# Optimization experiments

Measured on AMD Instinct MI355X. Metric: run time of the kernel, lower is better.

## Reference

```python
import jax, jax.numpy as jnp
import numpy as np
from jax import lax

ALPHA, BETA, THR = 0.9, 0.85, 1.0
NUM_STEPS = 100

@jax.custom_vjp
def spike(x):
    return (x > 0).astype(x.dtype)

def _spike_fwd(x):
    return (x > 0).astype(x.dtype), x

def _spike_bwd(x, g):
    # snntorch ATan surrogate (alpha=2.0): d spk / d x = 1 / (1 + (pi*x)^2)
    return (g / (1.0 + (jnp.pi * x) ** 2),)

spike.defvjp(_spike_fwd, _spike_bwd)

def setup_inputs() -> dict:
    key = jax.random.key(0)
    ks = jax.random.split(key, 5)
    B, IN, H, OUT = 8192, 784, 1000, 10
    x = jax.random.normal(ks[0], (B, IN), jnp.float32)
    s1 = 1.0 / float(np.sqrt(IN))
    s2 = 1.0 / float(np.sqrt(H))
    W1 = jax.random.uniform(ks[1], (H, IN), jnp.float32, -s1, s1)
    b1 = jax.random.uniform(ks[2], (H,), jnp.float32, -s1, s1)
    W2 = jax.random.uniform(ks[3], (OUT, H), jnp.float32, -s2, s2)
    b2 = jax.random.uniform(ks[4], (OUT,), jnp.float32, -s2, s2)
    return {"x": x, "W1": W1, "b1": b1, "W2": W2, "b2": b2}

def reference(x, W1, b1, W2, b2):
    # fc1 input is constant across all 100 steps, so the first GEMM is hoisted
    # out of the scan (identical math to recomputing it each step).
    cur1 = x @ W1.T + b1  # [B, H]
    B = x.shape[0]
    z1 = jnp.zeros((B, W1.shape[0]), x.dtype)
    z2 = jnp.zeros((B, W2.shape[0]), x.dtype)

    def step(carry, _):
        syn1, mem1, syn2, mem2 = carry
        # Synaptic LIF layer 1: reset uses detached spike of previous mem
        r1 = lax.stop_gradient((mem1 > THR).astype(x.dtype))
        syn1 = ALPHA * syn1 + cur1
        mem1 = BETA * mem1 + syn1 - r1 * THR
        spk1 = spike(mem1 - THR)
        cur2 = spk1 @ W2.T + b2  # [B, OUT]
        # Synaptic LIF layer 2
        r2 = lax.stop_gradient((mem2 > THR).astype(x.dtype))
        syn2 = ALPHA * syn2 + cur2
        mem2 = BETA * mem2 + syn2 - r2 * THR
        spk2 = spike(mem2 - THR)
        return (syn1, mem1, syn2, mem2), (spk2, mem2)

    _, (spk_rec, mem_rec) = lax.scan(step, (z1, z1, z2, z2), None, length=NUM_STEPS)
    return spk_rec, mem_rec  # each [100, B, 10]
```

## Files before the change

### kernel.cpp

```cpp
#include <hip/hip_runtime.h>
#include <stdint.h>

#define NB   8192
#define NIN  784
#define KP   800
#define NH   1000
#define NHP  1024
#define NOUT 10
#define NT   100

#define W2INV  4016.2227f
#define W2SCALE 2.4899824e-4f

typedef short bf16x8 __attribute__((ext_vector_type(8)));
typedef float f32x4  __attribute__((ext_vector_type(4)));
typedef int   i32x4  __attribute__((ext_vector_type(4)));


__device__ __forceinline__ uint16_t f2bf(float v) {
  uint32_t x = __float_as_uint(v);
  return (uint16_t)((x + 0x7FFFu + ((x >> 16) & 1u)) >> 16);
}

__global__ __launch_bounds__(256) void k_prep(
    const float* __restrict__ x, const float* __restrict__ W1,
    const float* __restrict__ W2,
    uint16_t* __restrict__ xh, uint16_t* __restrict__ xl,
    uint16_t* __restrict__ wh, uint16_t* __restrict__ wl,
    int8_t* __restrict__ w2i8) {
  const int bid = blockIdx.x;
  if (bid < 3600) {
    const float* src = (bid < 3200) ? x : W1;
    uint16_t* hi = (bid < 3200) ? xh : wh;
    uint16_t* lo = (bid < 3200) ? xl : wl;
    int rows_valid = (bid < 3200) ? NB : NH;
    int u = ((bid < 3200) ? bid : (bid - 3200)) * 256 + threadIdx.x;
    int lane = u & 63;
    int t = u >> 6;
    int kc = t % 25, blk = t / 25;
    int xx = lane & 15, g = lane >> 4;
    int row = blk * 16 + xx;
    int k0 = kc * 32 + g * 8;
    float4 a = {0, 0, 0, 0}, b = {0, 0, 0, 0};
    if (row < rows_valid && k0 + 8 <= NIN) {
      const float* p = src + (long)row * NIN + k0;
      a = *(const float4*)p;
      b = *(const float4*)(p + 4);
    }
    uint16_t h[8], l[8];
    float va[8] = {a.x, a.y, a.z, a.w, b.x, b.y, b.z, b.w};
#pragma unroll
    for (int j = 0; j < 8; ++j) {
      h[j] = f2bf(va[j]);
      float hv = __uint_as_float(((uint32_t)h[j]) << 16);
      l[j] = f2bf(va[j] - hv);
    }
    *(uint4*)(hi + (long)u * 8) = *(const uint4*)h;
    *(uint4*)(lo + (long)u * 8) = *(const uint4*)l;
  } else {
    int i = (bid - 3600) * 256 + threadIdx.x;
    int o = i >> 10, hh = i & 1023;
    float v = (o < NOUT && hh < NH) ? W2[o * NH + hh] : 0.0f;
    float q = rintf(v * W2INV);
    q = fmaxf(-127.0f, fminf(127.0f, q));
    w2i8[i] = (int8_t)(int)q;
  }
}

__global__ __launch_bounds__(256) void k_gemm1m(
    const uint16_t* __restrict__ xh, const uint16_t* __restrict__ xl,
    const uint16_t* __restrict__ wh, const uint16_t* __restrict__ wl,
    const float* __restrict__ b1, float* __restrict__ C) {
  const int lane = threadIdx.x & 63, w = threadIdx.x >> 6;
  const int x = lane & 15, g = lane >> 4;
  const int m0 = blockIdx.x << 6;
  const int n0 = (blockIdx.y << 8) + (w << 6);
  const int loff = lane << 3;
  long ab[4], bb[4];
#pragma unroll
  for (int s = 0; s < 4; ++s) {
    ab[s] = (long)((m0 >> 4) + s) * 12800 + loff;
    bb[s] = (long)((n0 >> 4) + s) * 12800 + loff;
  }
  f32x4 acc[4][4];
#pragma unroll
  for (int mt = 0; mt < 4; ++mt)
#pragma unroll
    for (int nt = 0; nt < 4; ++nt) acc[mt][nt] = (f32x4){0, 0, 0, 0};

#pragma unroll 5
  for (int kc = 0; kc < 25; ++kc) {
    const int ko = kc << 9;
    bf16x8 afh[4], afl[4], bfh[4], bfl[4];
#pragma unroll
    for (int s = 0; s < 4; ++s) {
      afh[s] = *(const bf16x8*)(xh + ab[s] + ko);
      afl[s] = *(const bf16x8*)(xl + ab[s] + ko);
      bfh[s] = *(const bf16x8*)(wh + bb[s] + ko);
      bfl[s] = *(const bf16x8*)(wl + bb[s] + ko);
    }
#pragma unroll
    for (int mt = 0; mt < 4; ++mt)
#pragma unroll
      for (int nt = 0; nt < 4; ++nt) {
        acc[mt][nt] = __builtin_amdgcn_mfma_f32_16x16x32_bf16(
            afh[mt], bfh[nt], acc[mt][nt], 0, 0, 0);
        acc[mt][nt] = __builtin_amdgcn_mfma_f32_16x16x32_bf16(
            afh[mt], bfl[nt], acc[mt][nt], 0, 0, 0);
        acc[mt][nt] = __builtin_amdgcn_mfma_f32_16x16x32_bf16(
            afl[mt], bfh[nt], acc[mt][nt], 0, 0, 0);
      }
  }
#pragma unroll
  for (int nt = 0; nt < 4; ++nt) {
    int n = n0 + (nt << 4) + x;
    if (n < NH) {
      float bias = b1[n];
#pragma unroll
      for (int mt = 0; mt < 4; ++mt)
#pragma unroll
        for (int r = 0; r < 4; ++r) {
          int m = m0 + (mt << 4) + (g << 2) + r;
          C[(long)m * NH + n] = acc[mt][nt][r] + bias;
        }
    }
  }
}

__global__ __launch_bounds__(256) void k_lif1(const float* __restrict__ cur1,
                                              uint32_t* __restrict__ spk32,
                                              uint16_t* __restrict__ spk16) {
  const int b = blockIdx.x, q = threadIdx.x;
  float4 c4 = {0, 0, 0, 0};
  if (q < 250) c4 = *(const float4*)(cur1 + (long)b * NH + (q << 2));
  float s0 = 0, s1 = 0, s2 = 0, s3 = 0;
  float m0 = 0, m1 = 0, m2 = 0, m3 = 0;
  float r0 = 0, r1 = 0, r2 = 0, r3 = 0;
  const float k9 = 0.9f, k85 = 0.85f, n1 = -1.0f;
  uint32_t* sp = spk32 + ((long)b << 8) + q;
  const long gstep = (long)NB << 8;
#define STEP(SH, BUF)                                                       \
  {                                                                         \
    float t0, t1, x0, x1, x2, x3;                                           \
    asm("v_fma_f32 %[s0], %[k9], %[s0], %[c0]\n\t"                          \
        "v_fma_f32 %[s1], %[k9], %[s1], %[c1]\n\t"                          \
        "v_fma_f32 %[s2], %[k9], %[s2], %[c2]\n\t"                          \
        "v_fma_f32 %[s3], %[k9], %[s3], %[c3]\n\t"                          \
        "v_add_f32 %[x0], %[s0], %[r0]\n\t"                                 \
        "v_add_f32 %[x1], %[s1], %[r1]\n\t"                                 \
        "v_add_f32 %[x2], %[s2], %[r2]\n\t"                                 \
        "v_add_f32 %[x3], %[s3], %[r3]\n\t"                                 \
        "v_fma_f32 %[m0], %[k85], %[m0], %[x0]\n\t"                         \
        "v_fma_f32 %[m1], %[k85], %[m1], %[x1]\n\t"                         \
        "v_fma_f32 %[m2], %[k85], %[m2], %[x2]\n\t"                         \
        "v_fma_f32 %[m3], %[k85], %[m3], %[x3]\n\t"                         \
        "v_cmp_lt_f32 vcc, 1.0, %[m0]\n\t"                                  \
        "v_cndmask_b32 %[r0], 0, %[n1], vcc\n\t"                            \
        "v_cmp_lt_f32 vcc, 1.0, %[m1]\n\t"                                  \
        "v_cndmask_b32 %[r1], 0, %[n1], vcc\n\t"                            \
        "v_cmp_lt_f32 vcc, 1.0, %[m2]\n\t"                                  \
        "v_cndmask_b32 %[r2], 0, %[n1], vcc\n\t"                            \
        "v_cmp_lt_f32 vcc, 1.0, %[m3]\n\t"                                  \
        "v_cndmask_b32 %[r3], 0, %[n1], vcc\n\t"                            \
        "v_fma_f32 %[t0], %[r1], -2.0, -%[r0]\n\t"                          \
        "v_fma_f32 %[t1], %[r3], -2.0, -%[r2]\n\t"                          \
        "v_fma_f32 %[t0], %[t1], 4.0, %[t0]\n\t"                            \
        "v_cvt_u32_f32 %[t1], %[t0]\n\t"                                    \
        "v_lshl_or_b32 %[buf], %[t1], " #SH ", %[buf]"                      \
        : [s0] "+v"(s0), [s1] "+v"(s1), [s2] "+v"(s2), [s3] "+v"(s3),       \
          [m0] "+v"(m0), [m1] "+v"(m1), [m2] "+v"(m2), [m3] "+v"(m3),       \
          [r0] "+v"(r0), [r1] "+v"(r1), [r2] "+v"(r2), [r3] "+v"(r3),       \
          [buf] "+v"(BUF), [t0] "=&v"(t0), [t1] "=&v"(t1),                  \
          [x0] "=&v"(x0), [x1] "=&v"(x1), [x2] "=&v"(x2), [x3] "=&v"(x3)    \
        : [c0] "v"(c4.x), [c1] "v"(c4.y), [c2] "v"(c4.z), [c3] "v"(c4.w),   \
          [k9] "v"(k9), [k85] "v"(k85), [n1] "v"(n1)                        \
        : "vcc");                                                           \
  }
  uint32_t bufA = 0, bufB = 0;
  for (int gi = 0; gi < 6; ++gi) {
    bufA = 0;
    STEP(0, bufA) STEP(4, bufA) STEP(8, bufA) STEP(12, bufA)
    STEP(16, bufA) STEP(20, bufA) STEP(24, bufA) STEP(28, bufA)
    *sp = bufA;  sp += gstep;
    bufB = 0;
    STEP(0, bufB) STEP(4, bufB) STEP(8, bufB) STEP(12, bufB)
    STEP(16, bufB) STEP(20, bufB) STEP(24, bufB) STEP(28, bufB)
    *sp = bufB;  sp += gstep;
  }
  bufA = 0;
  STEP(0, bufA) STEP(4, bufA) STEP(8, bufA) STEP(12, bufA)
  spk16[((long)b << 8) + q] = (uint16_t)bufA;
#undef STEP
}

__global__ __launch_bounds__(256) void k_fc2a(const uint32_t* __restrict__ spk,
                                              const int8_t* __restrict__ w2i8,
                                              const float* __restrict__ b2,
                                              float* __restrict__ cur2) {
  const int lane = threadIdx.x & 63, w = threadIdx.x >> 6;
  const int x = lane & 15, g = lane >> 4;
  const int wid = blockIdx.x * 4 + w;
  const int gq = wid >> 9;
  const int bb = (wid & 511) << 4;
  const int8_t* wb = w2i8 + (x << 10) + (g << 4);
  const uint32_t* s0 = spk + (((long)gq * NB + bb + x) << 8) + (g << 2);
  i32x4 acc[8];
#pragma unroll
  for (int t = 0; t < 8; ++t) acc[t] = (i32x4){0, 0, 0, 0};

#pragma unroll
  for (int kc = 0; kc < 16; ++kc) {
    uint4 d = *(const uint4*)(s0 + (kc << 4));
    i32x4 af = *(const i32x4*)(wb + (kc << 6));
#pragma unroll
    for (int t = 0; t < 8; ++t) {
      uint32_t w0 = (((d.x >> (4 * t)) & 0xFu) * 0x00204081u) & 0x01010101u;
      uint32_t w1 = (((d.y >> (4 * t)) & 0xFu) * 0x00204081u) & 0x01010101u;
      uint32_t w2 = (((d.z >> (4 * t)) & 0xFu) * 0x00204081u) & 0x01010101u;
      uint32_t w3 = (((d.w >> (4 * t)) & 0xFu) * 0x00204081u) & 0x01010101u;
      i32x4 bf = {(int)w0, (int)w1, (int)w2, (int)w3};
      acc[t] = __builtin_amdgcn_mfma_i32_16x16x64_i8(af, bf, acc[t], 0, 0, 0);
    }
  }
  float bias[4];
#pragma unroll
  for (int r = 0; r < 4; ++r) {
    int o = (g << 2) + r;
    bias[r] = (o < NOUT) ? b2[o] : 0.0f;
  }
  long row = bb + x;
#pragma unroll
  for (int t = 0; t < 8; ++t) {
    long tb = ((long)(gq * 8 + t) * NB + row) * NOUT;
#pragma unroll
    for (int r = 0; r < 4; ++r) {
      int o = (g << 2) + r;
      if (o < NOUT) cur2[tb + o] = W2SCALE * (float)acc[t][r] + bias[r];
    }
  }
}

__global__ __launch_bounds__(256) void k_fc2b(const uint32_t* __restrict__ spk16d,
                                              const int8_t* __restrict__ w2i8,
                                              const float* __restrict__ b2,
                                              float* __restrict__ cur2) {
  const int lane = threadIdx.x & 63, w = threadIdx.x >> 6;
  const int x = lane & 15, g = lane >> 4;
  const int wid = blockIdx.x * 4 + w;
  const int bb = wid << 4;
  const int8_t* wb = w2i8 + (x << 10) + (g << 4);
  const uint32_t* s0 = spk16d + ((long)(bb + x) << 7) + (g << 1);
  i32x4 acc[4];
#pragma unroll
  for (int t = 0; t < 4; ++t) acc[t] = (i32x4){0, 0, 0, 0};

#pragma unroll
  for (int kc = 0; kc < 16; ++kc) {
    uint2 d = *(const uint2*)(s0 + (kc << 3));
    i32x4 af = *(const i32x4*)(wb + (kc << 6));
#pragma unroll
    for (int t = 0; t < 4; ++t) {
      uint32_t w0 = (((d.x >> (4 * t)) & 0xFu) * 0x00204081u) & 0x01010101u;
      uint32_t w1 = (((d.x >> (16 + 4 * t)) & 0xFu) * 0x00204081u) & 0x01010101u;
      uint32_t w2 = (((d.y >> (4 * t)) & 0xFu) * 0x00204081u) & 0x01010101u;
      uint32_t w3 = (((d.y >> (16 + 4 * t)) & 0xFu) * 0x00204081u) & 0x01010101u;
      i32x4 bf = {(int)w0, (int)w1, (int)w2, (int)w3};
      acc[t] = __builtin_amdgcn_mfma_i32_16x16x64_i8(af, bf, acc[t], 0, 0, 0);
    }
  }
  float bias[4];
#pragma unroll
  for (int r = 0; r < 4; ++r) {
    int o = (g << 2) + r;
    bias[r] = (o < NOUT) ? b2[o] : 0.0f;
  }
  long row = bb + x;
#pragma unroll
  for (int t = 0; t < 4; ++t) {
    long tb = ((long)(96 + t) * NB + row) * NOUT;
#pragma unroll
    for (int r = 0; r < 4; ++r) {
      int o = (g << 2) + r;
      if (o < NOUT) cur2[tb + o] = W2SCALE * (float)acc[t][r] + bias[r];
    }
  }
}

__global__ __launch_bounds__(256) void k_lif2(float* io) {
  const int gid = blockIdx.x * 256 + threadIdx.x;
  float* sp = io + gid;
  float* mm = io + 8192000 + gid;
  float syn = 0.0f, mem = 0.0f;
  float c0 = sp[0], c1 = sp[81920], c2 = sp[2 * 81920], c3 = sp[3 * 81920];
  for (int t = 0; t < NT; t += 4) {
    float n0 = sp[(t + 4) * 81920], n1 = sp[(t + 5) * 81920];
    float n2 = sp[(t + 6) * 81920], n3 = sp[(t + 7) * 81920];
#define L2STEP(TT, CC)                                   \
    {                                                    \
      syn = fmaf(0.9f, syn, CC);                         \
      float r = (mem > 1.0f) ? 1.0f : 0.0f;              \
      mem = fmaf(0.85f, mem, syn) - r;                   \
      sp[(t + TT) * 81920] = (mem > 1.0f) ? 1.0f : 0.0f; \
      mm[(t + TT) * 81920] = mem;                        \
    }
    L2STEP(0, c0) L2STEP(1, c1) L2STEP(2, c2) L2STEP(3, c3)
#undef L2STEP
    c0 = n0; c1 = n1; c2 = n2; c3 = n3;
  }
}

extern "C" void kernel_launch(void* const* d_in, const int* in_sizes, int n_in,
                              void* d_out, int out_size, void* d_ws, size_t ws_size,
                              hipStream_t stream) {
  const float* x  = (const float*)d_in[0];
  const float* W1 = (const float*)d_in[1];
  const float* b1 = (const float*)d_in[2];
  const float* W2 = (const float*)d_in[3];
  const float* b2 = (const float*)d_in[4];
  float* out = (float*)d_out;
  float* memhalf = out + 8192000;

  uint32_t* spk32 = (uint32_t*)d_ws;
  uint32_t* spk16d = (uint32_t*)((char*)d_ws + 100663296);
  uint16_t* spk16 = (uint16_t*)spk16d;
  int8_t* w2i8 = (int8_t*)((char*)d_ws + 104857600);

  uint16_t* xh = (uint16_t*)d_out;
  uint16_t* xl = (uint16_t*)((char*)d_out + 13107200);
  uint16_t* wh = (uint16_t*)((char*)d_out + 26214400);
  uint16_t* wl = (uint16_t*)((char*)d_out + 27852800);

  k_prep<<<3664, 256, 0, stream>>>(x, W1, W2, xh, xl, wh, wl, w2i8);
  dim3 gg(128, 4);
  k_gemm1m<<<gg, 256, 0, stream>>>(xh, xl, wh, wl, b1, memhalf);
  k_lif1<<<NB, 256, 0, stream>>>(memhalf, spk32, spk16);
  k_fc2a<<<1536, 256, 0, stream>>>(spk32, w2i8, b2, out);
  k_fc2b<<<128, 256, 0, stream>>>(spk16d, w2i8, b2, out);
  k_lif2<<<320, 256, 0, stream>>>(out);
}
```

Measured before the change: 200.0 us.

## Factor LIF1 synaptic recurrence, merge fc2 kernels, batch LIF2 loads

The layer-1 synaptic current is rewritten as cur1 times a shared geometric scalar S (S = 0.9*S + 1), which drops four per-element FMAs and four adds per step to one scalar FMA plus four FMAs. The two fc2 kernels are merged into one launch that branches on block index, removing one launch and its tail. LIF2 now loads 25 timesteps per chunk up front to get more memory-level parallelism. The factored recurrence changes floating-point rounding slightly, which could flip spikes near the threshold.

```diff
diff --git a/kernel.cpp b/kernel.cpp
--- a/kernel.cpp
+++ b/kernel.cpp
@@ -133,7 +133,7 @@
   const int b = blockIdx.x, q = threadIdx.x;
   float4 c4 = {0, 0, 0, 0};
   if (q < 250) c4 = *(const float4*)(cur1 + (long)b * NH + (q << 2));
-  float s0 = 0, s1 = 0, s2 = 0, s3 = 0;
+  float S = 0.0f;
   float m0 = 0, m1 = 0, m2 = 0, m3 = 0;
   float r0 = 0, r1 = 0, r2 = 0, r3 = 0;
   const float k9 = 0.9f, k85 = 0.85f, n1 = -1.0f;
@@ -141,19 +141,16 @@
   const long gstep = (long)NB << 8;
 #define STEP(SH, BUF)                                                       \
   {                                                                         \
-    float t0, t1, x0, x1, x2, x3;                                           \
-    asm("v_fma_f32 %[s0], %[k9], %[s0], %[c0]\n\t"                          \
-        "v_fma_f32 %[s1], %[k9], %[s1], %[c1]\n\t"                          \
-        "v_fma_f32 %[s2], %[k9], %[s2], %[c2]\n\t"                          \
-        "v_fma_f32 %[s3], %[k9], %[s3], %[c3]\n\t"                          \
-        "v_add_f32 %[x0], %[s0], %[r0]\n\t"                                 \
-        "v_add_f32 %[x1], %[s1], %[r1]\n\t"                                 \
-        "v_add_f32 %[x2], %[s2], %[r2]\n\t"                                 \
-        "v_add_f32 %[x3], %[s3], %[r3]\n\t"                                 \
-        "v_fma_f32 %[m0], %[k85], %[m0], %[x0]\n\t"                         \
-        "v_fma_f32 %[m1], %[k85], %[m1], %[x1]\n\t"                         \
-        "v_fma_f32 %[m2], %[k85], %[m2], %[x2]\n\t"                         \
-        "v_fma_f32 %[m3], %[k85], %[m3], %[x3]\n\t"                         \
+    float t0, t1, ta, tb, tc, td;                                           \
+    asm("v_fma_f32 %[S], %[k9], %[S], 1.0\n\t"                              \
+        "v_fma_f32 %[ta], %[c0], %[S], %[r0]\n\t"                           \
+        "v_fma_f32 %[tb], %[c1], %[S], %[r1]\n\t"                           \
+        "v_fma_f32 %[tc], %[c2], %[S], %[r2]\n\t"                           \
+        "v_fma_f32 %[td], %[c3], %[S], %[r3]\n\t"                           \
+        "v_fma_f32 %[m0], %[k85], %[m0], %[ta]\n\t"                         \
+        "v_fma_f32 %[m1], %[k85], %[m1], %[tb]\n\t"                         \
+        "v_fma_f32 %[m2], %[k85], %[m2], %[tc]\n\t"                         \
+        "v_fma_f32 %[m3], %[k85], %[m3], %[td]\n\t"                         \
         "v_cmp_lt_f32 vcc, 1.0, %[m0]\n\t"                                  \
         "v_cndmask_b32 %[r0], 0, %[n1], vcc\n\t"                            \
         "v_cmp_lt_f32 vcc, 1.0, %[m1]\n\t"                                  \
@@ -167,11 +164,11 @@
         "v_fma_f32 %[t0], %[t1], 4.0, %[t0]\n\t"                            \
         "v_cvt_u32_f32 %[t1], %[t0]\n\t"                                    \
         "v_lshl_or_b32 %[buf], %[t1], " #SH ", %[buf]"                      \
-        : [s0] "+v"(s0), [s1] "+v"(s1), [s2] "+v"(s2), [s3] "+v"(s3),       \
+        : [S] "+v"(S),                                                      \
           [m0] "+v"(m0), [m1] "+v"(m1), [m2] "+v"(m2), [m3] "+v"(m3),       \
           [r0] "+v"(r0), [r1] "+v"(r1), [r2] "+v"(r2), [r3] "+v"(r3),       \
           [buf] "+v"(BUF), [t0] "=&v"(t0), [t1] "=&v"(t1),                  \
-          [x0] "=&v"(x0), [x1] "=&v"(x1), [x2] "=&v"(x2), [x3] "=&v"(x3)    \
+          [ta] "=&v"(ta), [tb] "=&v"(tb), [tc] "=&v"(tc), [td] "=&v"(td)    \
         : [c0] "v"(c4.x), [c1] "v"(c4.y), [c2] "v"(c4.z), [c3] "v"(c4.w),   \
           [k9] "v"(k9), [k85] "v"(k85), [n1] "v"(n1)                        \
         : "vcc");                                                           \
@@ -193,95 +190,82 @@
 #undef STEP
 }
 
-__global__ __launch_bounds__(256) void k_fc2a(const uint32_t* __restrict__ spk,
-                                              const int8_t* __restrict__ w2i8,
-                                              const float* __restrict__ b2,
-                                              float* __restrict__ cur2) {
+__global__ __launch_bounds__(256) void k_fc2(const uint32_t* __restrict__ spk,
+                                             const uint32_t* __restrict__ spk16d,
+                                             const int8_t* __restrict__ w2i8,
+                                             const float* __restrict__ b2,
+                                             float* __restrict__ cur2) {
   const int lane = threadIdx.x & 63, w = threadIdx.x >> 6;
   const int x = lane & 15, g = lane >> 4;
-  const int wid = blockIdx.x * 4 + w;
-  const int gq = wid >> 9;
-  const int bb = (wid & 511) << 4;
   const int8_t* wb = w2i8 + (x << 10) + (g << 4);
-  const uint32_t* s0 = spk + (((long)gq * NB + bb + x) << 8) + (g << 2);
-  i32x4 acc[8];
-#pragma unroll
-  for (int t = 0; t < 8; ++t) acc[t] = (i32x4){0, 0, 0, 0};
-
-#pragma unroll
-  for (int kc = 0; kc < 16; ++kc) {
-    uint4 d = *(const uint4*)(s0 + (kc << 4));
-    i32x4 af = *(const i32x4*)(wb + (kc << 6));
-#pragma unroll
-    for (int t = 0; t < 8; ++t) {
-      uint32_t w0 = (((d.x >> (4 * t)) & 0xFu) * 0x00204081u) & 0x01010101u;
-      uint32_t w1 = (((d.y >> (4 * t)) & 0xFu) * 0x00204081u) & 0x01010101u;
-      uint32_t w2 = (((d.z >> (4 * t)) & 0xFu) * 0x00204081u) & 0x01010101u;
-      uint32_t w3 = (((d.w >> (4 * t)) & 0xFu) * 0x00204081u) & 0x01010101u;
-      i32x4 bf = {(int)w0, (int)w1, (int)w2, (int)w3};
-      acc[t] = __builtin_amdgcn_mfma_i32_16x16x64_i8(af, bf, acc[t], 0, 0, 0);
-    }
-  }
   float bias[4];
 #pragma unroll
   for (int r = 0; r < 4; ++r) {
     int o = (g << 2) + r;
     bias[r] = (o < NOUT) ? b2[o] : 0.0f;
   }
-  long row = bb + x;
-#pragma unroll
-  for (int t = 0; t < 8; ++t) {
-    long tb = ((long)(gq * 8 + t) * NB + row) * NOUT;
-#pragma unroll
-    for (int r = 0; r < 4; ++r) {
-      int o = (g << 2) + r;
-      if (o < NOUT) cur2[tb + o] = W2SCALE * (float)acc[t][r] + bias[r];
-    }
-  }
-}
-
-__global__ __launch_bounds__(256) void k_fc2b(const uint32_t* __restrict__ spk16d,
-                                              const int8_t* __restrict__ w2i8,
-                                              const float* __restrict__ b2,
-                                              float* __restrict__ cur2) {
-  const int lane = threadIdx.x & 63, w = threadIdx.x >> 6;
-  const int x = lane & 15, g = lane >> 4;
-  const int wid = blockIdx.x * 4 + w;
-  const int bb = wid << 4;
-  const int8_t* wb = w2i8 + (x << 10) + (g << 4);
-  const uint32_t* s0 = spk16d + ((long)(bb + x) << 7) + (g << 1);
-  i32x4 acc[4];
-#pragma unroll
-  for (int t = 0; t < 4; ++t) acc[t] = (i32x4){0, 0, 0, 0};
-
-#pragma unroll
-  for (int kc = 0; kc < 16; ++kc) {
-    uint2 d = *(const uint2*)(s0 + (kc << 3));
-    i32x4 af = *(const i32x4*)(wb + (kc << 6));
+  if (blockIdx.x < 1536) {
+    const int wid = blockIdx.x * 4 + w;
+    const int gq = wid >> 9;
+    const int bb = (wid & 511) << 4;
+    const uint32_t* s0 = spk + (((long)gq * NB + bb + x) << 8) + (g << 2);
+    i32x4 acc[8];
+#pragma unroll
+    for (int t = 0; t < 8; ++t) acc[t] = (i32x4){0, 0, 0, 0};
+#pragma unroll
+    for (int kc = 0; kc < 16; ++kc) {
+      uint4 d = *(const uint4*)(s0 + (kc << 4));
+      i32x4 af = *(const i32x4*)(wb + (kc << 6));
+#pragma unroll
+      for (int t = 0; t < 8; ++t) {
+        uint32_t w0 = (((d.x >> (4 * t)) & 0xFu) * 0x00204081u) & 0x01010101u;
+        uint32_t w1 = (((d.y >> (4 * t)) & 0xFu) * 0x00204081u) & 0x01010101u;
+        uint32_t w2 = (((d.z >> (4 * t)) & 0xFu) * 0x00204081u) & 0x01010101u;
+        uint32_t w3 = (((d.w >> (4 * t)) & 0xFu) * 0x00204081u) & 0x01010101u;
+        i32x4 bf = {(int)w0, (int)w1, (int)w2, (int)w3};
+        acc[t] = __builtin_amdgcn_mfma_i32_16x16x64_i8(af, bf, acc[t], 0, 0, 0);
+      }
+    }
+    long row = bb + x;
+#pragma unroll
+    for (int t = 0; t < 8; ++t) {
+      long tb = ((long)(gq * 8 + t) * NB + row) * NOUT;
+#pragma unroll
+      for (int r = 0; r < 4; ++r) {
+        int o = (g << 2) + r;
+        if (o < NOUT) cur2[tb + o] = W2SCALE * (float)acc[t][r] + bias[r];
+      }
+    }
+  } else {
+    const int wid = (blockIdx.x - 1536) * 4 + w;
+    const int bb = wid << 4;
+    const uint32_t* s0 = spk16d + ((long)(bb + x) << 7) + (g << 1);
+    i32x4 acc[4];
+#pragma unroll
+    for (int t = 0; t < 4; ++t) acc[t] = (i32x4){0, 0, 0, 0};
+#pragma unroll
+    for (int kc = 0; kc < 16; ++kc) {
+      uint2 d = *(const uint2*)(s0 + (kc << 3));
+      i32x4 af = *(const i32x4*)(wb + (kc << 6));
+#pragma unroll
+      for (int t = 0; t < 4; ++t) {
+        uint32_t w0 = (((d.x >> (4 * t)) & 0xFu) * 0x00204081u) & 0x01010101u;
+        uint32_t w1 = (((d.x >> (16 + 4 * t)) & 0xFu) * 0x00204081u) & 0x01010101u;
+        uint32_t w2 = (((d.y >> (4 * t)) & 0xFu) * 0x00204081u) & 0x01010101u;
+        uint32_t w3 = (((d.y >> (16 + 4 * t)) & 0xFu) * 0x00204081u) & 0x01010101u;
+        i32x4 bf = {(int)w0, (int)w1, (int)w2, (int)w3};
+        acc[t] = __builtin_amdgcn_mfma_i32_16x16x64_i8(af, bf, acc[t], 0, 0, 0);
+      }
+    }
+    long row = bb + x;
 #pragma unroll
     for (int t = 0; t < 4; ++t) {
-      uint32_t w0 = (((d.x >> (4 * t)) & 0xFu) * 0x00204081u) & 0x01010101u;
-      uint32_t w1 = (((d.x >> (16 + 4 * t)) & 0xFu) * 0x00204081u) & 0x01010101u;
-      uint32_t w2 = (((d.y >> (4 * t)) & 0xFu) * 0x00204081u) & 0x01010101u;
-      uint32_t w3 = (((d.y >> (16 + 4 * t)) & 0xFu) * 0x00204081u) & 0x01010101u;
-      i32x4 bf = {(int)w0, (int)w1, (int)w2, (int)w3};
-      acc[t] = __builtin_amdgcn_mfma_i32_16x16x64_i8(af, bf, acc[t], 0, 0, 0);
-    }
-  }
-  float bias[4];
-#pragma unroll
-  for (int r = 0; r < 4; ++r) {
-    int o = (g << 2) + r;
-    bias[r] = (o < NOUT) ? b2[o] : 0.0f;
-  }
-  long row = bb + x;
-#pragma unroll
-  for (int t = 0; t < 4; ++t) {
-    long tb = ((long)(96 + t) * NB + row) * NOUT;
-#pragma unroll
-    for (int r = 0; r < 4; ++r) {
-      int o = (g << 2) + r;
-      if (o < NOUT) cur2[tb + o] = W2SCALE * (float)acc[t][r] + bias[r];
+      long tb = ((long)(96 + t) * NB + row) * NOUT;
+#pragma unroll
+      for (int r = 0; r < 4; ++r) {
+        int o = (g << 2) + r;
+        if (o < NOUT) cur2[tb + o] = W2SCALE * (float)acc[t][r] + bias[r];
+      }
     }
   }
 }
@@ -291,21 +275,21 @@
   float* sp = io + gid;
   float* mm = io + 8192000 + gid;
   float syn = 0.0f, mem = 0.0f;
-  float c0 = sp[0], c1 = sp[81920], c2 = sp[2 * 81920], c3 = sp[3 * 81920];
-  for (int t = 0; t < NT; t += 4) {
-    float n0 = sp[(t + 4) * 81920], n1 = sp[(t + 5) * 81920];
-    float n2 = sp[(t + 6) * 81920], n3 = sp[(t + 7) * 81920];
-#define L2STEP(TT, CC)                                   \
-    {                                                    \
-      syn = fmaf(0.9f, syn, CC);                         \
-      float r = (mem > 1.0f) ? 1.0f : 0.0f;              \
-      mem = fmaf(0.85f, mem, syn) - r;                   \
-      sp[(t + TT) * 81920] = (mem > 1.0f) ? 1.0f : 0.0f; \
-      mm[(t + TT) * 81920] = mem;                        \
-    }
-    L2STEP(0, c0) L2STEP(1, c1) L2STEP(2, c2) L2STEP(3, c3)
-#undef L2STEP
-    c0 = n0; c1 = n1; c2 = n2; c3 = n3;
+#pragma unroll 1
+  for (int ch = 0; ch < 4; ++ch) {
+    float* base = sp + (long)ch * 25 * 81920;
+    float* mbase = mm + (long)ch * 25 * 81920;
+    float c[25];
+#pragma unroll
+    for (int i = 0; i < 25; ++i) c[i] = base[(long)i * 81920];
+#pragma unroll
+    for (int i = 0; i < 25; ++i) {
+      syn = fmaf(0.9f, syn, c[i]);
+      float r = (mem > 1.0f) ? 1.0f : 0.0f;
+      mem = fmaf(0.85f, mem, syn) - r;
+      base[(long)i * 81920] = (mem > 1.0f) ? 1.0f : 0.0f;
+      mbase[(long)i * 81920] = mem;
+    }
   }
 }
 
@@ -334,7 +318,6 @@
   dim3 gg(128, 4);
   k_gemm1m<<<gg, 256, 0, stream>>>(xh, xl, wh, wl, b1, memhalf);
   k_lif1<<<NB, 256, 0, stream>>>(memhalf, spk32, spk16);
-  k_fc2a<<<1536, 256, 0, stream>>>(spk32, w2i8, b2, out);
-  k_fc2b<<<128, 256, 0, stream>>>(spk16d, w2i8, b2, out);
+  k_fc2<<<1664, 256, 0, stream>>>(spk32, spk16d, w2i8, b2, out);
   k_lif2<<<320, 256, 0, stream>>>(out);
 }
```

Measured after the change: 180.1 us (median of 2 runs). 1.11x faster.
